# Optimization experiments

Hardware: AMD Instinct MI355X
Metric: run time of the kernel (lower is better)

Reference implementation:

```python
import jax, jax.numpy as jnp
import numpy as np

B, L, C = 8, 2048, 512
CI = C // 2  # internal_units


def setup_inputs() -> dict:
    key = jax.random.key(0)
    ks = jax.random.split(key, 4)
    inputs = jax.random.normal(ks[0], (B, L, C), dtype=jnp.float32)
    # Conv1D kernel_size=1 == per-position linear; kernel_initializer='random_normal' (stddev 0.05)
    Wx = 0.05 * jax.random.normal(ks[1], (C, CI), dtype=jnp.float32)
    Wy = 0.05 * jax.random.normal(ks[2], (C, CI), dtype=jnp.float32)
    Wo = 0.05 * jax.random.normal(ks[3], (C, C), dtype=jnp.float32)
    bx = jnp.zeros((CI,), dtype=jnp.float32)
    by = jnp.zeros((CI,), dtype=jnp.float32)
    bo = jnp.zeros((C,), dtype=jnp.float32)
    return {"inputs": inputs, "Wx": Wx, "bx": bx, "Wy": Wy, "by": by, "Wo": Wo, "bo": bo}


def reference(inputs, Wx, bx, Wy, by, Wo, bo):
    # 1x1 conv projections (per-position linear layers with bias)
    x_proj = jnp.einsum('blc,ci->bli', inputs, Wx) + bx   # [B, L, Ci]
    y_proj = jnp.einsum('blc,ci->bli', inputs, Wy) + by   # [B, L, Ci]
    o_proj = jnp.einsum('blc,cd->bld', inputs, Wo) + bo   # [B, L, C]
    # scores: batched matmul x @ y^T -> [B, L, L]
    scores = jnp.einsum('bli,bmi->blm', x_proj, y_proj)
    # NOTE: softmax over axis=0 (the BATCH axis), as in the original module
    attn = jax.nn.softmax(scores, axis=0)
    s_dot = jnp.einsum('blm,bmc->blc', attn, o_proj)       # [B, L, C]
    return inputs + s_dot
```

## Files before the change

kernel.cpp:

```cpp
#include <hip/hip_runtime.h>


#define NB 8
#define NL 2048
#define NC 512
#define NCI 256

using f16x8 = __attribute__((ext_vector_type(8))) _Float16;
using f32x4 = __attribute__((ext_vector_type(4))) float;
typedef unsigned short u16;

__device__ __forceinline__ u16 f16b(float x) {
    _Float16 h = (_Float16)x;
    return __builtin_bit_cast(u16, h);
}
__device__ __forceinline__ float f16tof(u16 u) {
    return (float)__builtin_bit_cast(_Float16, u);
}
__device__ __forceinline__ void gload16(const void* g, void* l) {
    __builtin_amdgcn_global_load_lds((__attribute__((address_space(1))) void*)g,
                                     (__attribute__((address_space(3))) void*)l,
                                     16, 0, 0);
}

__global__ __launch_bounds__(256) void cvt_x_kernel(const float* __restrict__ X,
                                                    u16* __restrict__ Xf)
{
    size_t i = (size_t)blockIdx.x * 256 + threadIdx.x;
    const float4* X4 = (const float4*)X;
    float4 a = X4[2 * i], b = X4[2 * i + 1];
    u16 o[8] = {f16b(a.x), f16b(a.y), f16b(a.z), f16b(a.w),
                f16b(b.x), f16b(b.y), f16b(b.z), f16b(b.w)};
    ((uint4*)Xf)[i] = *(const uint4*)o;
}

__global__ __launch_bounds__(256) void cvt_w_kernel(
    const float* __restrict__ Wx, const float* __restrict__ Wy, const float* __restrict__ Wo,
    u16* __restrict__ WxT, u16* __restrict__ WyT, u16* __restrict__ WoT)
{
    const int bid = blockIdx.x, t = threadIdx.x;
#pragma unroll
    for (int kk = 0; kk < 2; ++kk) {
        const int k = t + kk * 256;
        if (bid < 256)      WxT[(size_t)bid * NC + k] = f16b(Wx[(size_t)k * NCI + bid]);
        else if (bid < 512) WyT[(size_t)(bid - 256) * NC + k] = f16b(Wy[(size_t)k * NCI + (bid - 256)]);
        else                WoT[(size_t)(bid - 512) * NC + k] = f16b(Wo[(size_t)k * NC + (bid - 512)]);
    }
}

__global__ __launch_bounds__(256) void proj_kernel(
    const u16* __restrict__ Xf,
    const u16* __restrict__ WxT, const u16* __restrict__ WyT, const u16* __restrict__ WoT,
    const float* __restrict__ bx, const float* __restrict__ by, const float* __restrict__ bo,
    u16* __restrict__ xp, u16* __restrict__ yp, u16* __restrict__ opT)
{
    __shared__ __align__(16) u16 SM[17408];
    u16* As = SM;
    u16* Bs = SM + 8192;

    const int tid = threadIdx.x;
    const int w = tid >> 6, lane = tid & 63;
    const int row0 = blockIdx.x * 128;
    const int cb = blockIdx.y;

    const u16* W; const float* bias; int n0, path;
    if (cb < 2)      { path = 0; n0 = cb * 128;       W = WxT; bias = bx; }
    else if (cb < 4) { path = 1; n0 = (cb - 2) * 128; W = WyT; bias = by; }
    else             { path = 2; n0 = (cb - 4) * 128; W = WoT; bias = bo; }

    f32x4 acc[4][4] = {};
    const int wm = (w & 1) * 64, wn = (w >> 1) * 64;
    const int fr = lane & 15, fq = lane >> 4;

    for (int k0 = 0; k0 < NC; k0 += 64) {
#pragma unroll
        for (int pass = 0; pass < 4; ++pass) {
            const int cbase = pass * 256 + w * 64;
            const int chunk = cbase + lane;
            const int r = chunk >> 3;
            const int kc = (chunk & 7) ^ (r & 7);
            gload16(Xf + (size_t)(row0 + r) * NC + k0 + kc * 8, (char*)As + cbase * 16);
            gload16(W  + (size_t)(n0  + r) * NC + k0 + kc * 8, (char*)Bs + cbase * 16);
        }
        __syncthreads();
        f16x8 a[4][2], b[4][2];
#pragma unroll
        for (int mi = 0; mi < 4; ++mi)
#pragma unroll
            for (int kt = 0; kt < 2; ++kt)
                a[mi][kt] = *(const f16x8*)&As[(wm + mi * 16 + fr) * 64 + ((kt * 4 + fq) ^ (fr & 7)) * 8];
#pragma unroll
        for (int ni = 0; ni < 4; ++ni)
#pragma unroll
            for (int kt = 0; kt < 2; ++kt)
                b[ni][kt] = *(const f16x8*)&Bs[(wn + ni * 16 + fr) * 64 + ((kt * 4 + fq) ^ (fr & 7)) * 8];
#pragma unroll
        for (int kt = 0; kt < 2; ++kt)
#pragma unroll
            for (int mi = 0; mi < 4; ++mi)
#pragma unroll
                for (int ni = 0; ni < 4; ++ni)
                    acc[mi][ni] = __builtin_amdgcn_mfma_f32_16x16x32_f16(a[mi][kt], b[ni][kt], acc[mi][ni], 0, 0, 0);
        __syncthreads();
    }

    if (path != 2) {
        u16* O = (path == 0) ? xp : yp;
#pragma unroll
        for (int mi = 0; mi < 4; ++mi) {
            const int grow = row0 + wm + mi * 16 + fq * 4;
#pragma unroll
            for (int ni = 0; ni < 4; ++ni) {
                const int gcol = n0 + wn + ni * 16 + fr;
                const float bv = bias[gcol];
#pragma unroll
                for (int r = 0; r < 4; ++r)
                    O[(size_t)(grow + r) * NCI + gcol] = f16b(acc[mi][ni][r] + bv);
            }
        }
    } else {
        u16* Ts = SM;
#pragma unroll
        for (int mi = 0; mi < 4; ++mi) {
            const int mb = wm + mi * 16 + fq * 4;
#pragma unroll
            for (int ni = 0; ni < 4; ++ni) {
                const int nl_ = wn + ni * 16 + fr;
                const float bv = bias[n0 + nl_];
#pragma unroll
                for (int r = 0; r < 4; ++r)
                    Ts[nl_ * 136 + mb + r] = f16b(acc[mi][ni][r] + bv);
            }
        }
        __syncthreads();
        const int b = row0 >> 11, m0 = row0 & 2047;
        u16* dst = opT + (size_t)b * NC * NL + (size_t)n0 * NL + m0;
        for (int i = tid; i < 128 * 16; i += 256) {
            const int c = i >> 4, ch = i & 15;
            uint4 v = *(const uint4*)&Ts[c * 136 + ch * 8];
            *(uint4*)&dst[(size_t)c * NL + ch * 8] = v;
        }
    }
}

__global__ __launch_bounds__(256) void score_softmax_kernel(
    const u16* __restrict__ xp, const u16* __restrict__ yp, u16* __restrict__ ATT)
{
    __shared__ __align__(16) u16 As[4096], Bs[4096];
    const int tid = threadIdx.x;
    const int w = tid >> 6, lane = tid & 63;
    const int row0 = blockIdx.x * 64, col0 = blockIdx.y * 64;
    const int wn = w * 16;
    const int fr = lane & 15, fq = lane >> 4;

    unsigned sv[NB][8];

#pragma unroll
    for (int b = 0; b < NB; ++b) {
        const u16* A = xp + (size_t)b * NL * NCI;
        const u16* B = yp + (size_t)b * NL * NCI;
        f32x4 acc[4] = {};
        for (int k0 = 0; k0 < NCI; k0 += 64) {
#pragma unroll
            for (int pass = 0; pass < 2; ++pass) {
                const int cbase = pass * 256 + w * 64;
                const int chunk = cbase + lane;
                const int r = chunk >> 3;
                const int kc = (chunk & 7) ^ (r & 7);
                gload16(A + (size_t)(row0 + r) * NCI + k0 + kc * 8, (char*)As + cbase * 16);
                gload16(B + (size_t)(col0 + r) * NCI + k0 + kc * 8, (char*)Bs + cbase * 16);
            }
            __syncthreads();
            f16x8 af[4][2], bf[2];
#pragma unroll
            for (int mi = 0; mi < 4; ++mi)
#pragma unroll
                for (int kt = 0; kt < 2; ++kt)
                    af[mi][kt] = *(const f16x8*)&As[(mi * 16 + fr) * 64 + ((kt * 4 + fq) ^ (fr & 7)) * 8];
#pragma unroll
            for (int kt = 0; kt < 2; ++kt)
                bf[kt] = *(const f16x8*)&Bs[(wn + fr) * 64 + ((kt * 4 + fq) ^ (fr & 7)) * 8];
#pragma unroll
            for (int kt = 0; kt < 2; ++kt)
#pragma unroll
                for (int mi = 0; mi < 4; ++mi)
                    acc[mi] = __builtin_amdgcn_mfma_f32_16x16x32_f16(af[mi][kt], bf[kt], acc[mi], 0, 0, 0);
            __syncthreads();
        }
#pragma unroll
        for (int mi = 0; mi < 4; ++mi) {
            sv[b][mi * 2 + 0] = (unsigned)f16b(acc[mi][0]) | ((unsigned)f16b(acc[mi][1]) << 16);
            sv[b][mi * 2 + 1] = (unsigned)f16b(acc[mi][2]) | ((unsigned)f16b(acc[mi][3]) << 16);
        }
    }

    const int gc = col0 + wn + fr;
#pragma unroll
    for (int mi = 0; mi < 4; ++mi) {
#pragma unroll
        for (int rp = 0; rp < 2; ++rp) {
            float v0[NB], v1[NB];
#pragma unroll
            for (int b = 0; b < NB; ++b) {
                unsigned u = sv[b][mi * 2 + rp];
                v0[b] = f16tof((u16)(u & 0xFFFF));
                v1[b] = f16tof((u16)(u >> 16));
            }
            float m0 = v0[0], m1 = v1[0];
#pragma unroll
            for (int b = 1; b < NB; ++b) { m0 = fmaxf(m0, v0[b]); m1 = fmaxf(m1, v1[b]); }
            float s0 = 0.f, s1 = 0.f;
#pragma unroll
            for (int b = 0; b < NB; ++b) {
                v0[b] = __expf(v0[b] - m0); s0 += v0[b];
                v1[b] = __expf(v1[b] - m1); s1 += v1[b];
            }
            const float i0 = 1.f / s0, i1 = 1.f / s1;
            const int gr0 = row0 + mi * 16 + fq * 4 + rp * 2;
#pragma unroll
            for (int b = 0; b < NB; ++b) {
                u16* dst = ATT + (size_t)b * NL * NL;
                dst[(size_t)gr0 * NL + gc]       = f16b(v0[b] * i0);
                dst[(size_t)(gr0 + 1) * NL + gc] = f16b(v1[b] * i1);
            }
        }
    }
}

__global__ __launch_bounds__(512) void out_kernel(
    const u16* __restrict__ ATT, const u16* __restrict__ opT,
    const float* __restrict__ X, float* __restrict__ Out)
{
    __shared__ __align__(16) u16 As[2][8192], Bs[2][8192];
    const int tid = threadIdx.x;
    const int w = tid >> 6, lane = tid & 63;
    const int b = blockIdx.z;
    const int row0 = blockIdx.x * 128, col0 = blockIdx.y * 128;
    const u16* Aatt = ATT + (size_t)b * NL * NL;
    const u16* Bsrc = opT + (size_t)b * NC * NL;

    f32x4 acc[4][2] = {};
    const int wm = (w & 1) * 64, wn = (w >> 1) * 32;
    const int fr = lane & 15, fq = lane >> 4;

    auto stage = [&](int k0, int bu) {
#pragma unroll
        for (int pass = 0; pass < 2; ++pass) {
            const int cbase = pass * 512 + w * 64;
            const int chunk = cbase + lane;
            const int r = chunk >> 3;
            const int kc = (chunk & 7) ^ (r & 7);
            gload16(Aatt + (size_t)(row0 + r) * NL + k0 + kc * 8, (char*)&As[bu][0] + cbase * 16);
            gload16(Bsrc + (size_t)(col0 + r) * NL + k0 + kc * 8, (char*)&Bs[bu][0] + cbase * 16);
        }
    };

    stage(0, 0);
    int bu = 0;
    for (int it = 0; it < NL / 64; ++it) {
        __syncthreads();
        if (it + 1 < NL / 64) stage((it + 1) * 64, bu ^ 1);
        f16x8 af[4][2], bf[2][2];
#pragma unroll
        for (int mi = 0; mi < 4; ++mi)
#pragma unroll
            for (int kt = 0; kt < 2; ++kt)
                af[mi][kt] = *(const f16x8*)&As[bu][(wm + mi * 16 + fr) * 64 + ((kt * 4 + fq) ^ (fr & 7)) * 8];
#pragma unroll
        for (int ni = 0; ni < 2; ++ni)
#pragma unroll
            for (int kt = 0; kt < 2; ++kt)
                bf[ni][kt] = *(const f16x8*)&Bs[bu][(wn + ni * 16 + fr) * 64 + ((kt * 4 + fq) ^ (fr & 7)) * 8];
#pragma unroll
        for (int kt = 0; kt < 2; ++kt)
#pragma unroll
            for (int mi = 0; mi < 4; ++mi)
#pragma unroll
                for (int ni = 0; ni < 2; ++ni)
                    acc[mi][ni] = __builtin_amdgcn_mfma_f32_16x16x32_f16(af[mi][kt], bf[ni][kt], acc[mi][ni], 0, 0, 0);
        bu ^= 1;
    }
    const size_t ob = (size_t)b * NL * NC;
#pragma unroll
    for (int mi = 0; mi < 4; ++mi) {
        const int gr = row0 + wm + mi * 16 + fq * 4;
#pragma unroll
        for (int ni = 0; ni < 2; ++ni) {
            const int gc = col0 + wn + ni * 16 + fr;
#pragma unroll
            for (int r = 0; r < 4; ++r) {
                const size_t o = ob + (size_t)(gr + r) * NC + gc;
                Out[o] = X[o] + acc[mi][ni][r];
            }
        }
    }
}

extern "C" void kernel_launch(void* const* d_in, const int* in_sizes, int n_in,
                              void* d_out, int out_size, void* d_ws, size_t ws_size,
                              hipStream_t stream)
{
    const float* X  = (const float*)d_in[0];
    const float* Wx = (const float*)d_in[1];
    const float* bx = (const float*)d_in[2];
    const float* Wy = (const float*)d_in[3];
    const float* by = (const float*)d_in[4];
    const float* Wo = (const float*)d_in[5];
    const float* bo = (const float*)d_in[6];
    float* out = (float*)d_out;

    char* ws = (char*)d_ws;
    u16* ATT = (u16*)ws;
    u16* Xf  = (u16*)ws;
    char* p = ws + 67108864;
    u16* xp  = (u16*)p; p += 8388608;
    u16* yp  = (u16*)p; p += 8388608;
    u16* opT = (u16*)p; p += 16777216;
    u16* WxT = (u16*)p; p += 262144;
    u16* WyT = (u16*)p; p += 262144;
    u16* WoT = (u16*)p; p += 524288;

    cvt_x_kernel<<<4096, 256, 0, stream>>>(X, Xf);
    cvt_w_kernel<<<1024, 256, 0, stream>>>(Wx, Wy, Wo, WxT, WyT, WoT);
    proj_kernel<<<dim3(128, 8), 256, 0, stream>>>(Xf, WxT, WyT, WoT, bx, by, bo, xp, yp, opT);
    score_softmax_kernel<<<dim3(32, 32), 256, 0, stream>>>(xp, yp, ATT);
    out_kernel<<<dim3(16, 4, NB), 512, 0, stream>>>(ATT, opT, X, out);
}
```

Baseline: 216.8 us.

## Load full K=256 score tiles into LDS per batch in one shot

The score kernel now stages the whole 64x256 x- and y-projection tiles for each batch into shared memory at once, instead of looping over four 64-wide K chunks with a barrier pair each. The XOR swizzle is widened to 32 chunks per row to match. The aim is fewer barriers and more loads in flight per batch. In exchange LDS use per block rises to 64 KB, which can cut occupancy, and the batch loop is no longer unrolled.

Result: slower. 221.5 us (+2.2%).

```diff
diff --git a/kernel.cpp b/kernel.cpp
--- a/kernel.cpp
+++ b/kernel.cpp
@@ -146,7 +146,7 @@
 __global__ __launch_bounds__(256) void score_softmax_kernel(
     const u16* __restrict__ xp, const u16* __restrict__ yp, u16* __restrict__ ATT)
 {
-    __shared__ __align__(16) u16 As[4096], Bs[4096];
+    __shared__ __align__(16) u16 As[64 * 256], Bs[64 * 256];
     const int tid = threadIdx.x;
     const int w = tid >> 6, lane = tid & 63;
     const int row0 = blockIdx.x * 64, col0 = blockIdx.y * 64;
@@ -155,38 +155,38 @@
 
     unsigned sv[NB][8];
 
-#pragma unroll
+#pragma unroll 1
     for (int b = 0; b < NB; ++b) {
         const u16* A = xp + (size_t)b * NL * NCI;
         const u16* B = yp + (size_t)b * NL * NCI;
+#pragma unroll
+        for (int pass = 0; pass < 8; ++pass) {
+            const int cbase = pass * 256 + w * 64;
+            const int chunk = cbase + lane;
+            const int r = chunk >> 5;
+            const int kc = (chunk & 31) ^ (r & 31);
+            gload16(A + (size_t)(row0 + r) * NCI + kc * 8, (char*)As + cbase * 16);
+            gload16(B + (size_t)(col0 + r) * NCI + kc * 8, (char*)Bs + cbase * 16);
+        }
+        __syncthreads();
         f32x4 acc[4] = {};
-        for (int k0 = 0; k0 < NCI; k0 += 64) {
-#pragma unroll
-            for (int pass = 0; pass < 2; ++pass) {
-                const int cbase = pass * 256 + w * 64;
-                const int chunk = cbase + lane;
-                const int r = chunk >> 3;
-                const int kc = (chunk & 7) ^ (r & 7);
-                gload16(A + (size_t)(row0 + r) * NCI + k0 + kc * 8, (char*)As + cbase * 16);
-                gload16(B + (size_t)(col0 + r) * NCI + k0 + kc * 8, (char*)Bs + cbase * 16);
-            }
-            __syncthreads();
-            f16x8 af[4][2], bf[2];
+#pragma unroll
+        for (int kt = 0; kt < 8; ++kt) {
+            f16x8 af[4], bf;
+#pragma unroll
+            for (int mi = 0; mi < 4; ++mi) {
+                const int row = mi * 16 + fr;
+                af[mi] = *(const f16x8*)&As[row * 256 + ((kt * 4 + fq) ^ (row & 31)) * 8];
+            }
+            {
+                const int row = wn + fr;
+                bf = *(const f16x8*)&Bs[row * 256 + ((kt * 4 + fq) ^ (row & 31)) * 8];
+            }
 #pragma unroll
             for (int mi = 0; mi < 4; ++mi)
-#pragma unroll
-                for (int kt = 0; kt < 2; ++kt)
-                    af[mi][kt] = *(const f16x8*)&As[(mi * 16 + fr) * 64 + ((kt * 4 + fq) ^ (fr & 7)) * 8];
-#pragma unroll
-            for (int kt = 0; kt < 2; ++kt)
-                bf[kt] = *(const f16x8*)&Bs[(wn + fr) * 64 + ((kt * 4 + fq) ^ (fr & 7)) * 8];
-#pragma unroll
-            for (int kt = 0; kt < 2; ++kt)
-#pragma unroll
-                for (int mi = 0; mi < 4; ++mi)
-                    acc[mi] = __builtin_amdgcn_mfma_f32_16x16x32_f16(af[mi][kt], bf[kt], acc[mi], 0, 0, 0);
-            __syncthreads();
-        }
+                acc[mi] = __builtin_amdgcn_mfma_f32_16x16x32_f16(af[mi], bf, acc[mi], 0, 0, 0);
+        }
+        __syncthreads();
 #pragma unroll
         for (int mi = 0; mi < 4; ++mi) {
             sv[b][mi * 2 + 0] = (unsigned)f16b(acc[mi][0]) | ((unsigned)f16b(acc[mi][1]) << 16);
```
